# Kernel tuning notes

Measured on AMD Instinct MI355X. Metric: run time of the kernel, lower is better.

The kernel has to match this reference:

```python
import jax, jax.numpy as jnp
import numpy as np

EMBED_DIM = 1024


def setup_inputs() -> dict:
    key = jax.random.key(0)
    ks = jax.random.split(key, 9)
    B, S, D = 4, 4096, EMBED_DIM
    s = 1.0 / np.sqrt(D)
    inp = {"x": jax.random.normal(ks[0], (B, S, D), dtype=jnp.float32)}
    names = ["q", "k", "v", "out"]
    for i, n in enumerate(names):
        inp[f"w_{n}"] = jax.random.uniform(ks[1 + 2 * i], (D, D), jnp.float32, -s, s)
        inp[f"b_{n}"] = jax.random.uniform(ks[2 + 2 * i], (D,), jnp.float32, -s, s)
    return inp


def reference(x, w_q, b_q, w_k, b_k, w_v, b_v, w_out, b_out):
    D = x.shape[-1]
    scaling = 1.0 / jnp.sqrt(jnp.asarray(D, x.dtype))
    q = jnp.einsum("bsd,ed->bse", x, w_q) + b_q
    k = jnp.einsum("bsd,ed->bse", x, w_k) + b_k
    v = jnp.einsum("bsd,ed->bse", x, w_v) + b_v
    # full [B, S, S] attention matrix, as in the original module
    scores = jnp.einsum("bqd,bkd->bqk", q, k) * scaling
    attn = jax.nn.softmax(scores, axis=-1)
    out = jnp.einsum("bqk,bkd->bqd", attn, v)
    return jnp.einsum("bsd,ed->bse", out, w_out) + b_out
```

## Files before the change

### kernel.cpp

```cpp
#include <hip/hip_runtime.h>
#include <hip/hip_bf16.h>

typedef __hip_bfloat16 bf16;
typedef __bf16 bf16x8 __attribute__((ext_vector_type(8)));
typedef float f32x4 __attribute__((ext_vector_type(4)));

#define B_ 4
#define S_ 4096
#define D_ 1024
#define BS_ 16384
#define N3_ 3072

__device__ __forceinline__ void gld_lds16(const void* g, void* l) {
    __builtin_amdgcn_global_load_lds(
        (const __attribute__((address_space(1))) void*)g,
        (__attribute__((address_space(3))) void*)l, 16, 0, 0);
}

__device__ __forceinline__ void cast4_one(const float* __restrict__ in,
                                          bf16* __restrict__ out, int i) {
    float4 v = ((const float4*)in)[i];
    union { ushort4 u; bf16 h[4]; } cv;
    cv.h[0] = __float2bfloat16(v.x);
    cv.h[1] = __float2bfloat16(v.y);
    cv.h[2] = __float2bfloat16(v.z);
    cv.h[3] = __float2bfloat16(v.w);
    ((ushort4*)out)[i] = cv.u;
}

__global__ __launch_bounds__(256) void prologue(
    const float* __restrict__ x, const float* __restrict__ wq,
    const float* __restrict__ wk, const float* __restrict__ wv,
    const float* __restrict__ wo, const float* __restrict__ bq,
    const float* __restrict__ bk, const float* __restrict__ bv,
    bf16* __restrict__ xb, bf16* __restrict__ Wc, bf16* __restrict__ Wo,
    float* __restrict__ bc, float* __restrict__ ls) {
    const int blk = blockIdx.x, tid = threadIdx.x;
    if (blk < 16384) {
        cast4_one(x, xb, blk * 256 + tid);
    } else if (blk < 20480) {
        int w = (blk - 16384) >> 10;
        int i = ((blk - 16384) & 1023) * 256 + tid;
        const float* src = (w == 0) ? wq : (w == 1) ? wk : (w == 2) ? wv : wo;
        bf16* dst = (w == 3) ? Wo : Wc + (long)w * D_ * D_;
        cast4_one(src, dst, i);
    } else if (blk < 20544) {
        ls[(blk - 20480) * 256 + tid] = 0.f;
    } else {
        for (int i = tid; i < N3_; i += 256)
            bc[i] = (i < 1024) ? bq[i] : (i < 2048) ? bk[i - 1024] : bv[i - 2048];
    }
}

__global__ __launch_bounds__(256) void transpose_v(const bf16* __restrict__ QKV,
                                                   bf16* __restrict__ VT) {
    __shared__ bf16 t[32][33];
    const int b = blockIdx.z;
    const bf16* Vb = QKV + (long)b * S_ * N3_ + 2048;
    bf16* VTb = VT + (long)b * D_ * S_;
    const int s0 = blockIdx.x * 32, d0 = blockIdx.y * 32;
    const int r = threadIdx.x >> 5, c = threadIdx.x & 31;
#pragma unroll
    for (int i = 0; i < 4; i++)
        t[r + i * 8][c] = Vb[(long)(s0 + r + i * 8) * N3_ + d0 + c];
    __syncthreads();
#pragma unroll
    for (int i = 0; i < 4; i++)
        VTb[(long)(d0 + r + i * 8) * S_ + s0 + c] = t[c][r + i * 8];
}

template <int EPI, int BM>
__global__ __launch_bounds__(256, 2) void gemm_nt(
    const bf16* __restrict__ A, int lda, long sA,
    const bf16* __restrict__ B, int ldb, long sB,
    void* __restrict__ Cout, int ldc, long sC,
    int K, const float* __restrict__ bias,
    float* __restrict__ rowsum, int sL, float scale) {
    constexpr int MI = BM / 32;
    __shared__ __align__(16) bf16 As[BM * 64];
    __shared__ __align__(16) bf16 Bs[128 * 64];
    const int tid = threadIdx.x;
    const int lane = tid & 63;
    const int wave = tid >> 6;
    const int bz = blockIdx.z;
    const int m0 = blockIdx.x * BM, n0 = blockIdx.y * 128;
    A += (long)bz * sA;
    B += (long)bz * sB;
    rowsum += (long)bz * sL;

    const int wr = (wave >> 1) * (BM / 2);
    const int wc = (wave & 1) * 64;
    const int fm = lane & 15;
    const int q4 = lane >> 4;
    const int sw = fm & 7;
    const int rd0 = ((q4 ^ sw) << 3);
    const int rd1 = (((4 + q4) ^ sw) << 3);

    f32x4 zero = {0.f, 0.f, 0.f, 0.f};
    f32x4 acc[MI][4];
#pragma unroll
    for (int i = 0; i < MI; i++)
#pragma unroll
        for (int j = 0; j < 4; j++) acc[i][j] = zero;

    for (int k0 = 0; k0 < K; k0 += 64) {
#pragma unroll
        for (int t = 0; t < BM / 32; t++) {
            int c = tid + t * 256;
            int row = c >> 3;
            int q = (((c & 7) ^ (row & 7)) << 3);
            gld_lds16(A + (long)(m0 + row) * lda + k0 + q, As + c * 8);
        }
#pragma unroll
        for (int t = 0; t < 4; t++) {
            int c = tid + t * 256;
            int row = c >> 3;
            int q = (((c & 7) ^ (row & 7)) << 3);
            gld_lds16(B + (long)(n0 + row) * ldb + k0 + q, Bs + c * 8);
        }
        __syncthreads();
#pragma unroll
        for (int kh = 0; kh < 2; kh++) {
            const int rdo = kh ? rd1 : rd0;
            bf16x8 af[MI], bfr[4];
#pragma unroll
            for (int i = 0; i < MI; i++)
                af[i] = *(const bf16x8*)(As + (wr + i * 16 + fm) * 64 + rdo);
#pragma unroll
            for (int j = 0; j < 4; j++)
                bfr[j] = *(const bf16x8*)(Bs + (wc + j * 16 + fm) * 64 + rdo);
#pragma unroll
            for (int i = 0; i < MI; i++)
#pragma unroll
                for (int j = 0; j < 4; j++)
                    acc[i][j] = __builtin_amdgcn_mfma_f32_16x16x32_bf16(
                        af[i], bfr[j], acc[i][j], 0, 0, 0);
        }
        __syncthreads();
    }

#pragma unroll
    for (int i = 0; i < MI; i++)
#pragma unroll
        for (int r = 0; r < 4; r++) {
            const int grow = m0 + wr + q4 * 4 + i * 16 + r;
            if constexpr (EPI == 0) {
#pragma unroll
                for (int j = 0; j < 4; j++) {
                    int gcol = n0 + wc + j * 16 + fm;
                    ((bf16*)Cout)[(long)bz * sC + (long)grow * ldc + gcol] =
                        __float2bfloat16(acc[i][j][r] + bias[gcol]);
                }
            } else if constexpr (EPI == 1) {
                float s = 0.f;
#pragma unroll
                for (int j = 0; j < 4; j++) {
                    int gcol = n0 + wc + j * 16 + fm;
                    float v = __expf(acc[i][j][r] * scale);
                    bf16 hv = __float2bfloat16(v);
                    ((bf16*)Cout)[(long)bz * sC + (long)grow * ldc + gcol] = hv;
                    s += __bfloat162float(hv);
                }
                s += __shfl_xor(s, 1, 16);
                s += __shfl_xor(s, 2, 16);
                s += __shfl_xor(s, 4, 16);
                s += __shfl_xor(s, 8, 16);
                if (fm == 0) atomicAdd(rowsum + grow, s);
            } else if constexpr (EPI == 2) {
                float inv = 1.0f / rowsum[grow];
#pragma unroll
                for (int j = 0; j < 4; j++) {
                    int gcol = n0 + wc + j * 16 + fm;
                    ((bf16*)Cout)[(long)bz * sC + (long)grow * ldc + gcol] =
                        __float2bfloat16(acc[i][j][r] * inv);
                }
            } else {
#pragma unroll
                for (int j = 0; j < 4; j++) {
                    int gcol = n0 + wc + j * 16 + fm;
                    ((float*)Cout)[(long)bz * sC + (long)grow * ldc + gcol] =
                        acc[i][j][r] + bias[gcol];
                }
            }
        }
}

extern "C" void kernel_launch(void* const* d_in, const int* in_sizes, int n_in,
                              void* d_out, int out_size, void* d_ws, size_t ws_size,
                              hipStream_t stream) {
    const float* x  = (const float*)d_in[0];
    const float* wq = (const float*)d_in[1];
    const float* bq = (const float*)d_in[2];
    const float* wk = (const float*)d_in[3];
    const float* bk = (const float*)d_in[4];
    const float* wv = (const float*)d_in[5];
    const float* bv = (const float*)d_in[6];
    const float* wo = (const float*)d_in[7];
    const float* bo = (const float*)d_in[8];
    (void)in_sizes; (void)n_in; (void)out_size; (void)ws_size;

    char* p = (char*)d_ws;
    bf16* Wc  = (bf16*)p;  p += (long)N3_ * D_ * 2;
    bf16* Wo  = (bf16*)p;  p += (long)D_ * D_ * 2;
    float* bc = (float*)p; p += N3_ * 4;
    bf16* QKV = (bf16*)p;  p += (long)BS_ * N3_ * 2;
    float* ls = (float*)p; p += (long)BS_ * 4;

    bf16* xb = (bf16*)d_out;
    bf16* VT = (bf16*)((char*)d_out + 33554432);
    bf16* E  = (bf16*)d_out;

    prologue<<<dim3(20545), 256, 0, stream>>>(x, wq, wk, wv, wo, bq, bk, bv,
                                              xb, Wc, Wo, bc, ls);

    gemm_nt<0, 128><<<dim3(BS_ / 128, N3_ / 128, 1), 256, 0, stream>>>(
        xb, D_, 0, Wc, D_, 0, QKV, N3_, 0, D_, bc, ls, 0, 1.f);

    transpose_v<<<dim3(S_ / 32, D_ / 32, B_), 256, 0, stream>>>(QKV, VT);

    for (int b = 0; b < B_; ++b) {
        const long qoff = (long)b * S_ * N3_;
        gemm_nt<1, 128><<<dim3(32, 32, 1), 256, 0, stream>>>(
            QKV + qoff, N3_, 0, QKV + qoff + 1024, N3_, 0,
            E, S_, 0, D_, nullptr, ls + b * S_, 0, 0.03125f);
        gemm_nt<2, 64><<<dim3(64, 8, 1), 256, 0, stream>>>(
            E, S_, 0, VT + (long)b * D_ * S_, S_, 0,
            QKV + qoff, N3_, 0, S_, nullptr, ls + b * S_, 0, 1.f);
    }

    gemm_nt<3, 128><<<dim3(BS_ / 128, D_ / 128, 1), 256, 0, stream>>>(
        QKV, N3_, 0, Wo, D_, 0, d_out, D_, 0, D_, bo, ls, 0, 1.f);
}
```

Measured before the change: 650.3 us.

## Batch attention GEMMs across batches when workspace allows larger score buffers

```diff
diff --git a/kernel.cpp b/kernel.cpp
--- a/kernel.cpp
+++ b/kernel.cpp
@@ -197,7 +197,7 @@
     const float* bv = (const float*)d_in[6];
     const float* wo = (const float*)d_in[7];
     const float* bo = (const float*)d_in[8];
-    (void)in_sizes; (void)n_in; (void)out_size; (void)ws_size;
+    (void)in_sizes; (void)n_in; (void)out_size;
 
     char* p = (char*)d_ws;
     bf16* Wc  = (bf16*)p;  p += (long)N3_ * D_ * 2;
@@ -207,8 +207,23 @@
     float* ls = (float*)p; p += (long)BS_ * 4;
 
     bf16* xb = (bf16*)d_out;
-    bf16* VT = (bf16*)((char*)d_out + 33554432);
-    bf16* E  = (bf16*)d_out;
+
+    const size_t base = 109129728UL;
+    int tier;
+    bf16 *VT, *E;
+    if (ws_size >= base + 134217728UL) {
+        tier = 2;
+        E  = (bf16*)p;
+        VT = (bf16*)((char*)d_out + 33554432);
+    } else if (ws_size >= base + 33554432UL) {
+        tier = 1;
+        VT = (bf16*)p;
+        E  = (bf16*)d_out;
+    } else {
+        tier = 0;
+        VT = (bf16*)((char*)d_out + 33554432);
+        E  = (bf16*)d_out;
+    }
 
     prologue<<<dim3(20545), 256, 0, stream>>>(x, wq, wk, wv, wo, bq, bk, bv,
                                               xb, Wc, Wo, bc, ls);
@@ -218,14 +233,35 @@
 
     transpose_v<<<dim3(S_ / 32, D_ / 32, B_), 256, 0, stream>>>(QKV, VT);
 
-    for (int b = 0; b < B_; ++b) {
-        const long qoff = (long)b * S_ * N3_;
-        gemm_nt<1, 128><<<dim3(32, 32, 1), 256, 0, stream>>>(
-            QKV + qoff, N3_, 0, QKV + qoff + 1024, N3_, 0,
-            E, S_, 0, D_, nullptr, ls + b * S_, 0, 0.03125f);
-        gemm_nt<2, 64><<<dim3(64, 8, 1), 256, 0, stream>>>(
-            E, S_, 0, VT + (long)b * D_ * S_, S_, 0,
-            QKV + qoff, N3_, 0, S_, nullptr, ls + b * S_, 0, 1.f);
+    if (tier == 2) {
+        gemm_nt<1, 128><<<dim3(32, 32, 4), 256, 0, stream>>>(
+            QKV, N3_, (long)S_ * N3_, QKV + 1024, N3_, (long)S_ * N3_,
+            E, S_, (long)S_ * S_, D_, nullptr, ls, S_, 0.03125f);
+        gemm_nt<2, 128><<<dim3(32, 8, 4), 256, 0, stream>>>(
+            E, S_, (long)S_ * S_, VT, S_, (long)D_ * S_,
+            QKV, N3_, (long)S_ * N3_, S_, nullptr, ls, S_, 1.f);
+    } else if (tier == 1) {
+        for (int pr = 0; pr < 2; ++pr) {
+            const long qoff = (long)(2 * pr) * S_ * N3_;
+            gemm_nt<1, 128><<<dim3(32, 32, 2), 256, 0, stream>>>(
+                QKV + qoff, N3_, (long)S_ * N3_,
+                QKV + qoff + 1024, N3_, (long)S_ * N3_,
+                E, S_, (long)S_ * S_, D_, nullptr, ls + 2 * pr * S_, S_, 0.03125f);
+            gemm_nt<2, 128><<<dim3(32, 8, 2), 256, 0, stream>>>(
+                E, S_, (long)S_ * S_,
+                VT + (long)(2 * pr) * D_ * S_, S_, (long)D_ * S_,
+                QKV + qoff, N3_, (long)S_ * N3_, S_, nullptr, ls + 2 * pr * S_, S_, 1.f);
+        }
+    } else {
+        for (int b = 0; b < B_; ++b) {
+            const long qoff = (long)b * S_ * N3_;
+            gemm_nt<1, 128><<<dim3(32, 32, 1), 256, 0, stream>>>(
+                QKV + qoff, N3_, 0, QKV + qoff + 1024, N3_, 0,
+                E, S_, 0, D_, nullptr, ls + b * S_, 0, 0.03125f);
+            gemm_nt<2, 64><<<dim3(64, 8, 1), 256, 0, stream>>>(
+                E, S_, 0, VT + (long)b * D_ * S_, S_, 0,
+                QKV + qoff, N3_, 0, S_, nullptr, ls + b * S_, 0, 1.f);
+        }
     }
 
     gemm_nt<3, 128><<<dim3(BS_ / 128, D_ / 128, 1), 256, 0, stream>>>(
```

New measurement: 591.6 us. 1.1x faster.
